# Optimization experiments

Hardware: AMD Instinct MI355X
Metric: run time of the kernel (lower is better)

Reference implementation:

```python
import jax, jax.numpy as jnp
import numpy as np
import math

HIDDEN = 1024
N_HEADS = 16
HEAD_DIM = HIDDEN // N_HEADS  # 64
B, S = 4, 8192


def setup_inputs() -> dict:
    key = jax.random.key(0)
    ks = jax.random.split(key, 5)
    scale = 1.0 / math.sqrt(HIDDEN)
    return {
        "hidden_states": jax.random.normal(ks[0], (B, S, HIDDEN), dtype=jnp.float32),
        "Wq": jax.random.normal(ks[1], (HIDDEN, HIDDEN), dtype=jnp.float32) * scale,
        "Wk": jax.random.normal(ks[2], (HIDDEN, HIDDEN), dtype=jnp.float32) * scale,
        "Wv": jax.random.normal(ks[3], (HIDDEN, HIDDEN), dtype=jnp.float32) * scale,
        "Wo": jax.random.normal(ks[4], (HIDDEN, HIDDEN), dtype=jnp.float32) * scale,
    }


def reference(hidden_states, Wq, Wk, Wv, Wo):
    b, s, _ = hidden_states.shape
    # nn.Linear(bias=False): y = x @ W.T
    q = (hidden_states @ Wq.T).reshape(b, s, N_HEADS, HEAD_DIM)
    k = (hidden_states @ Wk.T).reshape(b, s, N_HEADS, HEAD_DIM)
    v = (hidden_states @ Wv.T).reshape(b, s, N_HEADS, HEAD_DIM)
    # Faithful to source: NO transpose to (b,h,s,d); matmul contracts head_dim
    # per (batch, position), yielding [b, s, h, h] head-mixing weights.
    attn = jnp.einsum("bshd,bstd->bsht", q, k) / math.sqrt(HEAD_DIM)
    attn = jax.nn.softmax(attn, axis=-1)
    out = jnp.einsum("bsht,bstd->bshd", attn, v).reshape(b, s, HIDDEN)
    return out @ Wo.T
```

## Files before the change

### kernel.cpp

```cpp
#include <hip/hip_runtime.h>
#include <hip/hip_bf16.h>


typedef short bf16x8 __attribute__((ext_vector_type(8)));
typedef float f32x4  __attribute__((ext_vector_type(4)));

__device__ __forceinline__ float bf2f(short u) {
    union { unsigned int ui; float f; } cv;
    cv.ui = ((unsigned int)(unsigned short)u) << 16;
    return cv.f;
}
__device__ __forceinline__ short f2bf(float f) {
    __hip_bfloat16 h = __float2bfloat16(f);
    return *reinterpret_cast<short*>(&h);
}

__device__ __forceinline__ void gload_lds16(const void* g, void* lds) {
    const unsigned __attribute__((address_space(1)))* gp =
        reinterpret_cast<const unsigned __attribute__((address_space(1)))*>((unsigned long long)g);
    unsigned __attribute__((address_space(3)))* lp =
        reinterpret_cast<unsigned __attribute__((address_space(3)))*>(
            (unsigned int)(unsigned long long)lds);
    __builtin_amdgcn_global_load_lds(gp, lp, 16, 0, 0);
}

__global__ void detect_dtype(const unsigned* __restrict__ x, int* __restrict__ flag) {
    __shared__ int cnt;
    if (threadIdx.x == 0) cnt = 0;
    __syncthreads();
    int c = 0;
    for (int i = threadIdx.x; i < 4096; i += 256) {
        const unsigned u = x[(long)i * 4001 + 3];
        const unsigned b = (u >> 7) & 0xFF;
        c += (b >= 0x70 && b <= 0x87) ? 1 : 0;
    }
    atomicAdd(&cnt, c);
    __syncthreads();
    if (threadIdx.x == 0) *flag = (cnt > 2048) ? 0 : 1;
}

__global__ void convert_any(const void* __restrict__ src, long eoff,
                            short* __restrict__ dst, long n,
                            const int* __restrict__ flag) {
    const int f = *flag;
    const long step = (long)gridDim.x * blockDim.x * 8;
    for (long i = ((long)blockIdx.x * blockDim.x + threadIdx.x) * 8; i < n; i += step) {
        if (f) {
            const float* s = (const float*)src + eoff + i;
            const f32x4 a = *(const f32x4*)s;
            const f32x4 b = *(const f32x4*)(s + 4);
            bf16x8 o;
            o[0] = f2bf(a[0]); o[1] = f2bf(a[1]); o[2] = f2bf(a[2]); o[3] = f2bf(a[3]);
            o[4] = f2bf(b[0]); o[5] = f2bf(b[1]); o[6] = f2bf(b[2]); o[7] = f2bf(b[3]);
            *(bf16x8*)(dst + i) = o;
        } else {
            *(bf16x8*)(dst + i) = *(const bf16x8*)((const short*)src + eoff + i);
        }
    }
}

__device__ __forceinline__ void gemm256_core(const short* __restrict__ A,
                                             const short* __restrict__ W,
                                             void* __restrict__ C,
                                             const int* flag_fp32,
                                             long m0, int n0, short* lds) {
    constexpr int K = 1024, N = 1024;
    const int tid  = threadIdx.x;
    const int lane = tid & 63;
    const int wid  = tid >> 6;
    const int wm = wid >> 2, wn = wid & 3;

    short* A0 = lds;
    short* B0 = lds + 16384;
    short* A1 = lds + 32768;
    short* B1 = lds + 49152;

    const int srl = tid >> 3;
    const int kcs = (tid & 7) ^ (srl & 7);
    int aoff[4], boff[4];
    #pragma unroll
    for (int i = 0; i < 4; ++i) {
        const int row = i * 64 + srl;
        aoff[i] = (int)((m0 + row) * K + kcs * 8);
        boff[i] = (n0 + row) * K + kcs * 8;
    }
    const int ldsw = wid * 512;

    f32x4 acc[8][4] = {};

    #pragma unroll
    for (int i = 0; i < 4; ++i) gload_lds16(A + aoff[i], A0 + i * 4096 + ldsw);
    #pragma unroll
    for (int i = 0; i < 4; ++i) gload_lds16(W + boff[i], B0 + i * 4096 + ldsw);
    asm volatile("s_waitcnt vmcnt(0)" ::: "memory");
    __builtin_amdgcn_s_barrier();

    for (int t = 0; t < 16; ++t) {
        const int cur = t & 1;
        const short* rA = cur ? A1 : A0;
        const short* rB = cur ? B1 : B0;
        short* sA = cur ? A0 : A1;
        short* sB = cur ? B0 : B1;
        const int kadd = (t + 1) * 64;
        const bool more = (t < 15);

        #pragma unroll
        for (int ks = 0; ks < 2; ++ks) {
            const int kx8 = ((ks * 4 + (lane >> 4)) ^ (lane & 7)) * 8;
            bf16x8 af[8], bfr[4];
            #pragma unroll
            for (int m = 0; m < 8; ++m)
                af[m] = *(const bf16x8*)(rA + (wm * 128 + m * 16 + (lane & 15)) * 64 + kx8);
            #pragma unroll
            for (int n = 0; n < 4; ++n)
                bfr[n] = *(const bf16x8*)(rB + (wn * 64 + n * 16 + (lane & 15)) * 64 + kx8);
            __builtin_amdgcn_sched_barrier(0);
            __builtin_amdgcn_s_barrier();
            __builtin_amdgcn_sched_barrier(0);
            if (more) {
                if (ks == 0) {
                    #pragma unroll
                    for (int i = 0; i < 4; ++i)
                        gload_lds16(A + aoff[i] + kadd, sA + i * 4096 + ldsw);
                } else {
                    #pragma unroll
                    for (int i = 0; i < 4; ++i)
                        gload_lds16(W + boff[i] + kadd, sB + i * 4096 + ldsw);
                }
            }
            asm volatile("s_waitcnt lgkmcnt(0)" ::: "memory");
            __builtin_amdgcn_sched_barrier(0);
            __builtin_amdgcn_s_setprio(1);
            #pragma unroll
            for (int m = 0; m < 8; ++m)
                #pragma unroll
                for (int n = 0; n < 4; ++n)
                    acc[m][n] = __builtin_amdgcn_mfma_f32_16x16x32_bf16(
                                    af[m], bfr[n], acc[m][n], 0, 0, 0);
            __builtin_amdgcn_s_setprio(0);
            __builtin_amdgcn_sched_barrier(0);
            if (ks == 1) {
                asm volatile("s_waitcnt vmcnt(0)" ::: "memory");
                __builtin_amdgcn_s_barrier();
            }
        }
    }

    const int f = flag_fp32 ? *flag_fp32 : 0;
    #pragma unroll
    for (int mf = 0; mf < 8; ++mf) {
        #pragma unroll
        for (int nf = 0; nf < 4; ++nf) {
            const int  col   = n0 + wn * 64 + nf * 16 + (lane & 15);
            const long rbase = m0 + wm * 128 + mf * 16 + (lane >> 4) * 4;
            if (f) {
                float* Cf = (float*)C;
                #pragma unroll
                for (int r = 0; r < 4; ++r)
                    Cf[(rbase + r) * N + col] = acc[mf][nf][r];
            } else {
                short* Cs = (short*)C;
                #pragma unroll
                for (int r = 0; r < 4; ++r)
                    Cs[(rbase + r) * N + col] = f2bf(acc[mf][nf][r]);
            }
        }
    }
}

__global__ __launch_bounds__(512, 2) void gemm_qkv256(const short* __restrict__ A,
                                                      const short* __restrict__ W0,
                                                      const short* __restrict__ W1,
                                                      const short* __restrict__ W2,
                                                      short* __restrict__ C0,
                                                      short* __restrict__ C1,
                                                      short* __restrict__ C2) {
    __shared__ __align__(16) short lds[65536];
    const int nwg = gridDim.x;
    const int q8  = nwg >> 3;
    const int d   = blockIdx.x;
    const int lin = (d & 7) * q8 + (d >> 3);
    const int x   = lin / 12;
    const int r   = lin - x * 12;
    const int yy  = r / 3;
    const int z   = r - yy * 3;
    const short* W = (z == 0) ? W0 : (z == 1) ? W1 : W2;
    short*       C = (z == 0) ? C0 : (z == 1) ? C1 : C2;
    gemm256_core(A, W, C, nullptr, (long)x * 256, yy * 256, lds);
}

__global__ __launch_bounds__(512, 2) void gemm_out256(const short* __restrict__ A,
                                                      const short* __restrict__ W,
                                                      void* __restrict__ C,
                                                      long moff,
                                                      const int* __restrict__ flag) {
    __shared__ __align__(16) short lds[65536];
    const int nwg = gridDim.x;
    const int q8  = nwg >> 3;
    const int d   = blockIdx.x;
    const int lin = (d & 7) * q8 + (d >> 3);
    const int x   = lin >> 2;
    const int yy  = lin & 3;
    gemm256_core(A, W, C, flag, moff + (long)x * 256, yy * 256, lds);
}

__global__ __launch_bounds__(256) void attn_mix(const short* __restrict__ Q,
                                                const short* __restrict__ K,
                                                const short* __restrict__ V,
                                                short* __restrict__ Z) {
    constexpr int RS = 72;
    __shared__ short sq[4][16 * RS];
    __shared__ short sk[4][16 * RS];
    __shared__ short sv[4][16 * RS];
    __shared__ float sp[4][256];

    const int  tid  = threadIdx.x;
    const int  lane = tid & 63;
    const int  w    = tid >> 6;
    const long tok  = (long)blockIdx.x * 4 + w;

    const short* qg = Q + tok * 1024;
    const short* kg = K + tok * 1024;
    const short* vg = V + tok * 1024;

    #pragma unroll
    for (int it = 0; it < 2; ++it) {
        const int c   = lane + 64 * it;
        const int row = c >> 3;
        const int cc  = (c & 7) * 8;
        *(bf16x8*)&sq[w][row * RS + cc] = *(const bf16x8*)(qg + c * 8);
        *(bf16x8*)&sk[w][row * RS + cc] = *(const bf16x8*)(kg + c * 8);
        *(bf16x8*)&sv[w][row * RS + cc] = *(const bf16x8*)(vg + c * 8);
    }
    __syncthreads();

    const int h  = lane >> 2;
    const int t0 = (lane & 3) * 4;
    float sc[4] = {0.f, 0.f, 0.f, 0.f};
    for (int d = 0; d < 64; ++d) {
        const float qv = bf2f(sq[w][h * RS + d]);
        #pragma unroll
        for (int j = 0; j < 4; ++j)
            sc[j] += qv * bf2f(sk[w][(t0 + j) * RS + d]);
    }
    #pragma unroll
    for (int j = 0; j < 4; ++j) sc[j] *= 0.125f;

    float mx = fmaxf(fmaxf(sc[0], sc[1]), fmaxf(sc[2], sc[3]));
    mx = fmaxf(mx, __shfl_xor(mx, 1));
    mx = fmaxf(mx, __shfl_xor(mx, 2));
    float ex[4], s = 0.f;
    #pragma unroll
    for (int j = 0; j < 4; ++j) { ex[j] = __expf(sc[j] - mx); s += ex[j]; }
    s += __shfl_xor(s, 1);
    s += __shfl_xor(s, 2);
    const float inv = 1.f / s;
    #pragma unroll
    for (int j = 0; j < 4; ++j) sp[w][h * 16 + t0 + j] = ex[j] * inv;
    __syncthreads();

    const int dbase = (lane & 3) * 16;
    float o[16] = {};
    for (int t = 0; t < 16; ++t) {
        const float p = sp[w][h * 16 + t];
        const bf16x8 v0 = *(const bf16x8*)&sv[w][t * RS + dbase];
        const bf16x8 v1 = *(const bf16x8*)&sv[w][t * RS + dbase + 8];
        #pragma unroll
        for (int e = 0; e < 8; ++e) {
            o[e]     += p * bf2f(v0[e]);
            o[e + 8] += p * bf2f(v1[e]);
        }
    }
    bf16x8 ov0, ov1;
    #pragma unroll
    for (int e = 0; e < 8; ++e) { ov0[e] = f2bf(o[e]); ov1[e] = f2bf(o[e + 8]); }
    *(bf16x8*)(Z + tok * 1024 + lane * 16)     = ov0;
    *(bf16x8*)(Z + tok * 1024 + lane * 16 + 8) = ov1;
}

extern "C" void kernel_launch(void* const* d_in, const int* in_sizes, int n_in,
                              void* d_out, int out_size, void* d_ws, size_t ws_size,
                              hipStream_t stream) {
    const void* X = d_in[0];

    const long TOT = 32768;
    constexpr long WELEM = 1024 * 1024;

    char* ws   = (char*)d_ws;
    int*  flag = (int*)ws;
    short* Wqb = (short*)(ws + 256);
    short* Wkb = Wqb + WELEM;
    short* Wvb = Wkb + WELEM;
    short* Wob = Wvb + WELEM;
    short* dyn = Wob + WELEM;

    const size_t fixed = 256 + 4 * WELEM * 2;
    long chunk = 256;
    const long tiers[4] = {32768, 8192, 2048, 512};
    for (int i = 0; i < 4; ++i)
        if (fixed + (size_t)6 * tiers[i] * 1024 * 2 <= ws_size) { chunk = tiers[i]; break; }

    short* Xb = dyn;
    short* Qb = Xb + chunk * 1024;
    short* Kb = Qb + chunk * 1024;
    short* Vb = Kb + chunk * 1024;
    short* Zb = Vb + chunk * 1024;

    detect_dtype<<<1, 256, 0, stream>>>((const unsigned*)X, flag);
    convert_any<<<512, 256, 0, stream>>>(d_in[1], 0, Wqb, WELEM, flag);
    convert_any<<<512, 256, 0, stream>>>(d_in[2], 0, Wkb, WELEM, flag);
    convert_any<<<512, 256, 0, stream>>>(d_in[3], 0, Wvb, WELEM, flag);
    convert_any<<<512, 256, 0, stream>>>(d_in[4], 0, Wob, WELEM, flag);

    for (long t0 = 0; t0 < TOT; t0 += chunk) {
        convert_any<<<2048, 256, 0, stream>>>(X, t0 * 1024, Xb, chunk * 1024, flag);
        gemm_qkv256<<<dim3((chunk / 256) * 12), 512, 0, stream>>>(Xb, Wqb, Wkb, Wvb,
                                                                  Qb, Kb, Vb);
        attn_mix<<<dim3(chunk / 4), 256, 0, stream>>>(Qb, Kb, Vb, Zb);
        gemm_out256<<<dim3((chunk / 256) * 4), 512, 0, stream>>>(Zb - t0 * 1024, Wob,
                                                                 d_out, t0, flag);
    }
}
```

Before: 415.5 us.

## Interleave second k-slice LDS reads with first-slice MFMAs and drop mid-tile barrier

Measured after the change: 427.8 us. +3.0%, slower.

```diff
diff --git a/kernel.cpp b/kernel.cpp
--- a/kernel.cpp
+++ b/kernel.cpp
@@ -94,6 +94,12 @@
     for (int i = 0; i < 4; ++i) gload_lds16(W + boff[i], B0 + i * 4096 + ldsw);
     asm volatile("s_waitcnt vmcnt(0)" ::: "memory");
     __builtin_amdgcn_s_barrier();
+    __builtin_amdgcn_sched_barrier(0);
+
+    const int arow = wm * 128 + (lane & 15);
+    const int brow = wn * 64 + (lane & 15);
+    const int kx0 = (((lane >> 4)) ^ (lane & 7)) * 8;
+    const int kx1 = ((4 + (lane >> 4)) ^ (lane & 7)) * 8;
 
     for (int t = 0; t < 16; ++t) {
         const int cur = t & 1;
@@ -104,45 +110,44 @@
         const int kadd = (t + 1) * 64;
         const bool more = (t < 15);
 
-        #pragma unroll
-        for (int ks = 0; ks < 2; ++ks) {
-            const int kx8 = ((ks * 4 + (lane >> 4)) ^ (lane & 7)) * 8;
-            bf16x8 af[8], bfr[4];
+        bf16x8 af0[8], bf0[4], af1[8], bf1[4];
+        #pragma unroll
+        for (int m = 0; m < 8; ++m)
+            af0[m] = *(const bf16x8*)(rA + (arow + m * 16) * 64 + kx0);
+        #pragma unroll
+        for (int n = 0; n < 4; ++n)
+            bf0[n] = *(const bf16x8*)(rB + (brow + n * 16) * 64 + kx0);
+        if (more) {
             #pragma unroll
-            for (int m = 0; m < 8; ++m)
-                af[m] = *(const bf16x8*)(rA + (wm * 128 + m * 16 + (lane & 15)) * 64 + kx8);
+            for (int i = 0; i < 4; ++i)
+                gload_lds16(A + aoff[i] + kadd, sA + i * 4096 + ldsw);
+            #pragma unroll
+            for (int i = 0; i < 4; ++i)
+                gload_lds16(W + boff[i] + kadd, sB + i * 4096 + ldsw);
+        }
+        __builtin_amdgcn_s_setprio(1);
+        #pragma unroll
+        for (int m = 0; m < 8; ++m) {
+            af1[m] = *(const bf16x8*)(rA + (arow + m * 16) * 64 + kx1);
+            if (m >= 4)
+                bf1[m - 4] = *(const bf16x8*)(rB + (brow + (m - 4) * 16) * 64 + kx1);
             #pragma unroll
             for (int n = 0; n < 4; ++n)
-                bfr[n] = *(const bf16x8*)(rB + (wn * 64 + n * 16 + (lane & 15)) * 64 + kx8);
-            __builtin_amdgcn_sched_barrier(0);
+                acc[m][n] = __builtin_amdgcn_mfma_f32_16x16x32_bf16(
+                                af0[m], bf0[n], acc[m][n], 0, 0, 0);
+        }
+        #pragma unroll
+        for (int m = 0; m < 8; ++m)
+            #pragma unroll
+            for (int n = 0; n < 4; ++n)
+                acc[m][n] = __builtin_amdgcn_mfma_f32_16x16x32_bf16(
+                                af1[m], bf1[n], acc[m][n], 0, 0, 0);
+        __builtin_amdgcn_s_setprio(0);
+        __builtin_amdgcn_sched_barrier(0);
+        if (more) {
+            asm volatile("s_waitcnt vmcnt(0)" ::: "memory");
             __builtin_amdgcn_s_barrier();
             __builtin_amdgcn_sched_barrier(0);
-            if (more) {
-                if (ks == 0) {
-                    #pragma unroll
-                    for (int i = 0; i < 4; ++i)
-                        gload_lds16(A + aoff[i] + kadd, sA + i * 4096 + ldsw);
-                } else {
-                    #pragma unroll
-                    for (int i = 0; i < 4; ++i)
-                        gload_lds16(W + boff[i] + kadd, sB + i * 4096 + ldsw);
-                }
-            }
-            asm volatile("s_waitcnt lgkmcnt(0)" ::: "memory");
-            __builtin_amdgcn_sched_barrier(0);
-            __builtin_amdgcn_s_setprio(1);
-            #pragma unroll
-            for (int m = 0; m < 8; ++m)
-                #pragma unroll
-                for (int n = 0; n < 4; ++n)
-                    acc[m][n] = __builtin_amdgcn_mfma_f32_16x16x32_bf16(
-                                    af[m], bfr[n], acc[m][n], 0, 0, 0);
-            __builtin_amdgcn_s_setprio(0);
-            __builtin_amdgcn_sched_barrier(0);
-            if (ks == 1) {
-                asm volatile("s_waitcnt vmcnt(0)" ::: "memory");
-                __builtin_amdgcn_s_barrier();
-            }
         }
     }
 
```

## Restructure GEMM main loop into four-quadrant phases with finer-grained async staging

Applied to the files above, without the earlier changes.

New measurement: 461.5 us. 1.11x slower.

```diff
diff --git a/kernel.cpp b/kernel.cpp
--- a/kernel.cpp
+++ b/kernel.cpp
@@ -70,80 +70,142 @@
     const int wid  = tid >> 6;
     const int wm = wid >> 2, wn = wid & 3;
 
+    const int srl = tid >> 3;
+    const int kcs = (tid & 7) ^ (srl & 7);
+    int aoff[4], boff[4];
+    #pragma unroll
+    for (int i = 0; i < 4; ++i) {
+        const int row = i * 64 + srl;
+        aoff[i] = (int)((m0 + row) * K + kcs * 8);
+        boff[i] = (n0 + row) * K + kcs * 8;
+    }
+    const int ldsw = wid * 512;
+
+    auto STAGE_HALF = [&](int u) {
+        if (u >= 64) return;
+        const int T = u >> 2, P = u & 3;
+        short* base = lds + (T & 1) * 32768;
+        const int kadd = T * 64;
+        if (P < 2) {
+            const int g = P * 2;
+            gload_lds16(A + aoff[g]     + kadd, base + g * 4096 + ldsw);
+            gload_lds16(A + aoff[g + 1] + kadd, base + (g + 1) * 4096 + ldsw);
+        } else {
+            const int g = (P - 2) * 2;
+            gload_lds16(W + boff[g]     + kadd, base + 16384 + g * 4096 + ldsw);
+            gload_lds16(W + boff[g + 1] + kadd, base + 16384 + (g + 1) * 4096 + ldsw);
+        }
+    };
+
+    f32x4 acc[8][4] = {};
+
+    const int arow = wm * 128 + (lane & 15);
+    const int brow = wn * 64 + (lane & 15);
+    const int kx0 = (((lane >> 4)) ^ (lane & 7)) * 8;
+    const int kx1 = ((4 + (lane >> 4)) ^ (lane & 7)) * 8;
+
+    #pragma unroll
+    for (int u = 0; u < 5; ++u) STAGE_HALF(u);
+    asm volatile("s_waitcnt vmcnt(2)" ::: "memory");
+    __builtin_amdgcn_s_barrier();
+    __builtin_amdgcn_sched_barrier(0);
+
+    auto TILE = [&](const short* rA, const short* rB, int t) {
+        const int su = 4 * t + 5;
+        bf16x8 a[8], b0r[4], b1r[4];
+        #pragma unroll
+        for (int m = 0; m < 4; ++m) {
+            a[2 * m]     = *(const bf16x8*)(rA + (arow + m * 16) * 64 + kx0);
+            a[2 * m + 1] = *(const bf16x8*)(rA + (arow + m * 16) * 64 + kx1);
+        }
+        #pragma unroll
+        for (int n = 0; n < 2; ++n) {
+            b0r[2 * n]     = *(const bf16x8*)(rB + (brow + n * 16) * 64 + kx0);
+            b0r[2 * n + 1] = *(const bf16x8*)(rB + (brow + n * 16) * 64 + kx1);
+        }
+        STAGE_HALF(su);
+        __builtin_amdgcn_sched_barrier(0);
+        __builtin_amdgcn_s_barrier();
+        asm volatile("s_waitcnt lgkmcnt(0)" ::: "memory");
+        __builtin_amdgcn_sched_barrier(0);
+        __builtin_amdgcn_s_setprio(1);
+        #pragma unroll
+        for (int m = 0; m < 4; ++m)
+            #pragma unroll
+            for (int n = 0; n < 2; ++n) {
+                acc[m][n] = __builtin_amdgcn_mfma_f32_16x16x32_bf16(a[2 * m],     b0r[2 * n],     acc[m][n], 0, 0, 0);
+                acc[m][n] = __builtin_amdgcn_mfma_f32_16x16x32_bf16(a[2 * m + 1], b0r[2 * n + 1], acc[m][n], 0, 0, 0);
+            }
+        __builtin_amdgcn_s_setprio(0);
+        __builtin_amdgcn_sched_barrier(0);
+        __builtin_amdgcn_s_barrier();
+        #pragma unroll
+        for (int n = 0; n < 2; ++n) {
+            b1r[2 * n]     = *(const bf16x8*)(rB + (brow + 32 + n * 16) * 64 + kx0);
+            b1r[2 * n + 1] = *(const bf16x8*)(rB + (brow + 32 + n * 16) * 64 + kx1);
+        }
+        STAGE_HALF(su + 1);
+        __builtin_amdgcn_sched_barrier(0);
+        __builtin_amdgcn_s_barrier();
+        asm volatile("s_waitcnt lgkmcnt(0)" ::: "memory");
+        __builtin_amdgcn_sched_barrier(0);
+        __builtin_amdgcn_s_setprio(1);
+        #pragma unroll
+        for (int m = 0; m < 4; ++m)
+            #pragma unroll
+            for (int n = 0; n < 2; ++n) {
+                acc[m][2 + n] = __builtin_amdgcn_mfma_f32_16x16x32_bf16(a[2 * m],     b1r[2 * n],     acc[m][2 + n], 0, 0, 0);
+                acc[m][2 + n] = __builtin_amdgcn_mfma_f32_16x16x32_bf16(a[2 * m + 1], b1r[2 * n + 1], acc[m][2 + n], 0, 0, 0);
+            }
+        __builtin_amdgcn_s_setprio(0);
+        __builtin_amdgcn_sched_barrier(0);
+        __builtin_amdgcn_s_barrier();
+        #pragma unroll
+        for (int m = 0; m < 4; ++m) {
+            a[2 * m]     = *(const bf16x8*)(rA + (arow + 64 + m * 16) * 64 + kx0);
+            a[2 * m + 1] = *(const bf16x8*)(rA + (arow + 64 + m * 16) * 64 + kx1);
+        }
+        STAGE_HALF(su + 2);
+        __builtin_amdgcn_sched_barrier(0);
+        __builtin_amdgcn_s_barrier();
+        asm volatile("s_waitcnt lgkmcnt(0)" ::: "memory");
+        __builtin_amdgcn_sched_barrier(0);
+        __builtin_amdgcn_s_setprio(1);
+        #pragma unroll
+        for (int m = 0; m < 4; ++m)
+            #pragma unroll
+            for (int n = 0; n < 2; ++n) {
+                acc[4 + m][n] = __builtin_amdgcn_mfma_f32_16x16x32_bf16(a[2 * m],     b0r[2 * n],     acc[4 + m][n], 0, 0, 0);
+                acc[4 + m][n] = __builtin_amdgcn_mfma_f32_16x16x32_bf16(a[2 * m + 1], b0r[2 * n + 1], acc[4 + m][n], 0, 0, 0);
+            }
+        __builtin_amdgcn_s_setprio(0);
+        __builtin_amdgcn_sched_barrier(0);
+        __builtin_amdgcn_s_barrier();
+        STAGE_HALF(su + 3);
+        if (t < 14)      asm volatile("s_waitcnt vmcnt(2)" ::: "memory");
+        else if (t == 14) asm volatile("s_waitcnt vmcnt(0)" ::: "memory");
+        __builtin_amdgcn_sched_barrier(0);
+        __builtin_amdgcn_s_barrier();
+        __builtin_amdgcn_s_setprio(1);
+        #pragma unroll
+        for (int m = 0; m < 4; ++m)
+            #pragma unroll
+            for (int n = 0; n < 2; ++n) {
+                acc[4 + m][2 + n] = __builtin_amdgcn_mfma_f32_16x16x32_bf16(a[2 * m],     b1r[2 * n],     acc[4 + m][2 + n], 0, 0, 0);
+                acc[4 + m][2 + n] = __builtin_amdgcn_mfma_f32_16x16x32_bf16(a[2 * m + 1], b1r[2 * n + 1], acc[4 + m][2 + n], 0, 0, 0);
+            }
+        __builtin_amdgcn_s_setprio(0);
+        __builtin_amdgcn_sched_barrier(0);
+        __builtin_amdgcn_s_barrier();
+    };
+
     short* A0 = lds;
     short* B0 = lds + 16384;
     short* A1 = lds + 32768;
     short* B1 = lds + 49152;
-
-    const int srl = tid >> 3;
-    const int kcs = (tid & 7) ^ (srl & 7);
-    int aoff[4], boff[4];
-    #pragma unroll
-    for (int i = 0; i < 4; ++i) {
-        const int row = i * 64 + srl;
-        aoff[i] = (int)((m0 + row) * K + kcs * 8);
-        boff[i] = (n0 + row) * K + kcs * 8;
-    }
-    const int ldsw = wid * 512;
-
-    f32x4 acc[8][4] = {};
-
-    #pragma unroll
-    for (int i = 0; i < 4; ++i) gload_lds16(A + aoff[i], A0 + i * 4096 + ldsw);
-    #pragma unroll
-    for (int i = 0; i < 4; ++i) gload_lds16(W + boff[i], B0 + i * 4096 + ldsw);
-    asm volatile("s_waitcnt vmcnt(0)" ::: "memory");
-    __builtin_amdgcn_s_barrier();
-
-    for (int t = 0; t < 16; ++t) {
-        const int cur = t & 1;
-        const short* rA = cur ? A1 : A0;
-        const short* rB = cur ? B1 : B0;
-        short* sA = cur ? A0 : A1;
-        short* sB = cur ? B0 : B1;
-        const int kadd = (t + 1) * 64;
-        const bool more = (t < 15);
-
-        #pragma unroll
-        for (int ks = 0; ks < 2; ++ks) {
-            const int kx8 = ((ks * 4 + (lane >> 4)) ^ (lane & 7)) * 8;
-            bf16x8 af[8], bfr[4];
-            #pragma unroll
-            for (int m = 0; m < 8; ++m)
-                af[m] = *(const bf16x8*)(rA + (wm * 128 + m * 16 + (lane & 15)) * 64 + kx8);
-            #pragma unroll
-            for (int n = 0; n < 4; ++n)
-                bfr[n] = *(const bf16x8*)(rB + (wn * 64 + n * 16 + (lane & 15)) * 64 + kx8);
-            __builtin_amdgcn_sched_barrier(0);
-            __builtin_amdgcn_s_barrier();
-            __builtin_amdgcn_sched_barrier(0);
-            if (more) {
-                if (ks == 0) {
-                    #pragma unroll
-                    for (int i = 0; i < 4; ++i)
-                        gload_lds16(A + aoff[i] + kadd, sA + i * 4096 + ldsw);
-                } else {
-                    #pragma unroll
-                    for (int i = 0; i < 4; ++i)
-                        gload_lds16(W + boff[i] + kadd, sB + i * 4096 + ldsw);
-                }
-            }
-            asm volatile("s_waitcnt lgkmcnt(0)" ::: "memory");
-            __builtin_amdgcn_sched_barrier(0);
-            __builtin_amdgcn_s_setprio(1);
-            #pragma unroll
-            for (int m = 0; m < 8; ++m)
-                #pragma unroll
-                for (int n = 0; n < 4; ++n)
-                    acc[m][n] = __builtin_amdgcn_mfma_f32_16x16x32_bf16(
-                                    af[m], bfr[n], acc[m][n], 0, 0, 0);
-            __builtin_amdgcn_s_setprio(0);
-            __builtin_amdgcn_sched_barrier(0);
-            if (ks == 1) {
-                asm volatile("s_waitcnt vmcnt(0)" ::: "memory");
-                __builtin_amdgcn_s_barrier();
-            }
-        }
+    for (int tt = 0; tt < 8; ++tt) {
+        TILE(A0, B0, tt * 2);
+        TILE(A1, B1, tt * 2 + 1);
     }
 
     const int f = flag_fp32 ? *flag_fp32 : 0;
```
